# Kernel tuning notes

Hardware: AMD Instinct MI355X
Metric: run time of the kernel (lower is better)

The kernel has to match this reference:

```python
import jax, jax.numpy as jnp
import numpy as np
from jax import lax

K = 3          # dynamic filter kernel size
NH = 8         # attention heads

def _conv2d(x, w, b, pad, groups=1):
    y = lax.conv_general_dilated(x, w, (1, 1), [(pad, pad), (pad, pad)],
                                 feature_group_count=groups,
                                 dimension_numbers=('NCHW', 'OIHW', 'NCHW'))
    return y + b[None, :, None, None]

def _pw(x, w, b):  # 1x1 conv: w (O,C)
    return jnp.einsum('oc,bchw->bohw', w, x) + b[None, :, None, None]

def _lrelu(x):
    return jnp.where(x >= 0, x, 0.2 * x)

def _unfold(x, k):  # (B,C,H,W) -> (B,C,k*k,H,W), matches F.unfold ordering
    p = k // 2
    xp = jnp.pad(x, ((0, 0), (0, 0), (p, p), (p, p)))
    H, W = x.shape[2], x.shape[3]
    return jnp.stack([xp[:, :, i:i + H, j:j + W] for i in range(k) for j in range(k)], axis=2)

def setup_inputs() -> dict:
    key = jax.random.key(0)
    ks = jax.random.split(key, 24)
    B, C, H, W = 1, 256, 56, 56
    C2, K2 = C // 2, K * K
    s = 0.02
    d = {
        'dec_feat': jax.random.normal(ks[0], (B, C, H, W), jnp.float32),
        'enc_feat': jax.random.normal(ks[1], (B, C, H, W), jnp.float32),
        # ALPF kernel predictor: depthwise 3x3, 1x1 C->C/2, 1x1 C/2->k^2
        'alpf_dw_w': jax.random.normal(ks[2], (C, 1, 3, 3), jnp.float32) * s,
        'alpf_dw_b': jnp.zeros((C,), jnp.float32),
        'alpf_p1_w': jax.random.normal(ks[3], (C2, C), jnp.float32) * s,
        'alpf_p1_b': jnp.zeros((C2,), jnp.float32),
        'alpf_p2_w': jax.random.normal(ks[4], (K2, C2), jnp.float32) * s,
        'alpf_p2_b': jnp.zeros((K2,), jnp.float32),
        # AHPF weight predictor: 3x3 C->C/2, 1x1 C/2->k^2
        'ahpf_c1_w': jax.random.normal(ks[5], (C2, C, 3, 3), jnp.float32) * s,
        'ahpf_c1_b': jnp.zeros((C2,), jnp.float32),
        'ahpf_c2_w': jax.random.normal(ks[6], (K2, C2), jnp.float32) * s,
        'ahpf_c2_b': jnp.zeros((K2,), jnp.float32),
        # cross-attention projections (all 1x1)
        'q_w': jax.random.normal(ks[7], (C, C), jnp.float32) * s,
        'q_b': jnp.zeros((C,), jnp.float32),
        'kv_w': jax.random.normal(ks[8], (2 * C, C), jnp.float32) * s,
        'kv_b': jnp.zeros((2 * C,), jnp.float32),
        'out_w': jax.random.normal(ks[9], (C, C), jnp.float32) * s,
        'out_b': jnp.zeros((C,), jnp.float32),
        # fusion 3x3 conv
        'fusion_w': jax.random.normal(ks[10], (C, C, 3, 3), jnp.float32) * s,
        'fusion_b': jnp.zeros((C,), jnp.float32),
    }
    return d

def _forward(dec_feat, enc_feat, alpf_dw_w, alpf_dw_b, alpf_p1_w, alpf_p1_b,
             alpf_p2_w, alpf_p2_b, ahpf_c1_w, ahpf_c1_b, ahpf_c2_w, ahpf_c2_b,
             q_w, q_b, kv_w, kv_b, out_w, out_b, fusion_w, fusion_b):
    B, C, H, W = dec_feat.shape
    K2 = K * K
    # ---- Adaptive low-pass filter on dec_feat ----
    kw = _conv2d(dec_feat, alpf_dw_w, alpf_dw_b, pad=1, groups=C)
    kw = _lrelu(_pw(kw, alpf_p1_w, alpf_p1_b))
    kw = _pw(kw, alpf_p2_w, alpf_p2_b)            # (B,k2,H,W)
    kw = jax.nn.softmax(kw, axis=1)
    patches = _unfold(dec_feat, K)                # (B,C,k2,H,W)
    f_smooth = jnp.sum(patches * kw[:, None], axis=2)
    # ---- Cross attention: q from f_smooth, kv from enc_feat ----
    hd = C // NH
    N = H * W
    q = _pw(f_smooth, q_w, q_b).reshape(B, NH, hd, N)
    kv = _pw(enc_feat, kv_w, kv_b)
    k, v = jnp.split(kv, 2, axis=1)
    k = k.reshape(B, NH, hd, N)
    v = v.reshape(B, NH, hd, N)
    scale = hd ** -0.5
    attn = jnp.einsum('bhdn,bhdm->bhnm', q, k) * scale
    attn = jax.nn.softmax(attn, axis=-1)
    out = jnp.einsum('bhnm,bhdm->bhdn', attn, v).reshape(B, C, H, W)
    f_aligned = _pw(out, out_w, out_b)
    # ---- Adaptive high-pass filter on enc_feat ----
    wlp = _lrelu(_conv2d(enc_feat, ahpf_c1_w, ahpf_c1_b, pad=1))
    wlp = jax.nn.softmax(_pw(wlp, ahpf_c2_w, ahpf_c2_b), axis=1)  # (B,k2,H,W)
    whp = (-wlp).at[:, K2 // 2].add(1.0)          # delta - W_LP
    epatches = _unfold(enc_feat, K)
    f_high = enc_feat + jnp.sum(epatches * whp[:, None], axis=2)
    # ---- Fusion (w = 1.0) ----
    return _conv2d(f_aligned + 1.0 * f_high, fusion_w, fusion_b, pad=1)

def reference(dec_feat, enc_feat, alpf_dw_w, alpf_dw_b, alpf_p1_w, alpf_p1_b,
              alpf_p2_w, alpf_p2_b, ahpf_c1_w, ahpf_c1_b, ahpf_c2_w, ahpf_c2_b,
              q_w, q_b, kv_w, kv_b, out_w, out_b, fusion_w, fusion_b):
    return _forward(dec_feat, enc_feat, alpf_dw_w, alpf_dw_b, alpf_p1_w, alpf_p1_b,
                    alpf_p2_w, alpf_p2_b, ahpf_c1_w, ahpf_c1_b, ahpf_c2_w, ahpf_c2_b,
                    q_w, q_b, kv_w, kv_b, out_w, out_b, fusion_w, fusion_b)
```

## Files before the change

kernel.cpp:

```cpp
#include <hip/hip_runtime.h>
#include <hip/hip_bf16.h>

#define HH  56
#define WWC 56
#define HWP 3136
#define CC  256
#define NSPLIT 6

typedef unsigned short u16;
typedef __attribute__((ext_vector_type(8))) u16 u16x8;
typedef __attribute__((ext_vector_type(4))) u16 u16x4;
typedef __attribute__((ext_vector_type(8))) short s16x8;
typedef __attribute__((ext_vector_type(4))) float f32x4;

__device__ __forceinline__ u16 f2b(float f) {
  unsigned int x = __float_as_uint(f);
  return (u16)((x + 0x7fffu + ((x >> 16) & 1u)) >> 16);
}
__device__ __forceinline__ float b2f(u16 u) {
  return __uint_as_float(((unsigned int)u) << 16);
}
__device__ __forceinline__ f32x4 mfma16(s16x8 a, s16x8 b, f32x4 c) {
  return __builtin_amdgcn_mfma_f32_16x16x32_bf16(a, b, c, 0, 0, 0);
}

__device__ __forceinline__ float ldsel(const void* p, int i, bool bf) {
  if (bf) return __bfloat162float(((const __hip_bfloat16*)p)[i]);
  return ((const float*)p)[i];
}
__device__ __forceinline__ void stsel(void* p, int i, float v, bool bf) {
  if (bf) ((__hip_bfloat16*)p)[i] = __float2bfloat16(v);
  else ((float*)p)[i] = v;
}

__device__ __forceinline__ void ldrow8(const void* p, size_t i, bool bf,
                                       float* o) {
  if (bf) {
    u16x8 v = *(const u16x8*)((const u16*)p + i);
    #pragma unroll
    for (int j = 0; j < 8; ++j) o[j] = b2f(v[j]);
  } else {
    const float* f = (const float*)p + i;
    f32x4 a = *(const f32x4*)f;
    f32x4 b = *(const f32x4*)(f + 4);
    #pragma unroll
    for (int j = 0; j < 4; ++j) { o[j] = a[j]; o[4 + j] = b[j]; }
  }
}

__global__ void detect_dtype_k(const void* x, float* flag) {
  __shared__ int sh[256];
  int tid = threadIdx.x;
  const __hip_bfloat16* xb = (const __hip_bfloat16*)x;
  int ok = 0;
  for (int i = tid; i < 1024; i += 256) {
    float v = fabsf(__bfloat162float(xb[2 * i]));
    if (v > 9.5e-7f && v < 1.05e6f) ok++;
  }
  sh[tid] = ok;
  __syncthreads();
  for (int s = 128; s > 0; s >>= 1) {
    if (tid < s) sh[tid] += sh[tid + s];
    __syncthreads();
  }
  if (tid == 0) flag[0] = (sh[0] > 512) ? 1.f : 0.f;
}

__global__ __launch_bounds__(256)
void pack_all_k(const void* __restrict__ p1, const void* __restrict__ q,
                const void* __restrict__ kv, const void* __restrict__ ow,
                const void* __restrict__ c1, const void* __restrict__ fu,
                u16* __restrict__ d_p1, u16* __restrict__ d_q,
                u16* __restrict__ d_kv, u16* __restrict__ d_ow,
                u16* __restrict__ d_c1, u16* __restrict__ d_fu,
                const float* __restrict__ dflag) {
  bool bf = dflag[0] > 0.5f;
  int b = blockIdx.x, tid = threadIdx.x;
  if (b < 128) { int g = b * 256 + tid; d_p1[g] = f2b(ldsel(p1, g, bf)); return; }
  b -= 128;
  if (b < 256) { int g = b * 256 + tid; d_q[g] = f2b(ldsel(q, g, bf)); return; }
  b -= 256;
  if (b < 512) { int g = b * 256 + tid; d_kv[g] = f2b(ldsel(kv, g, bf)); return; }
  b -= 512;
  if (b < 256) { int g = b * 256 + tid; d_ow[g] = f2b(ldsel(ow, g, bf)); return; }
  b -= 256;
  if (b < 128) {
    int g = b * 256 + tid;
    #pragma unroll
    for (int t = 0; t < 9; ++t)
      d_c1[(size_t)t * 32768 + g] = f2b(ldsel(c1, g * 9 + t, bf));
    return;
  }
  b -= 128;
  {
    int g = b * 256 + tid;
    #pragma unroll
    for (int t = 0; t < 9; ++t)
      d_fu[(size_t)t * 65536 + g] = f2b(ldsel(fu, g * 9 + t, bf));
  }
}

__device__ __forceinline__ void dwconv_body(int gid, const void* x,
                                            const void* wt, const void* bs,
                                            u16* y, bool bf) {
  int c = gid / 392, g = gid - c * 392;
  int p0 = g * 8;
  int h = p0 / WWC, w0 = p0 - h * WWC;
  float wv[9];
  #pragma unroll
  for (int t = 0; t < 9; ++t) wv[t] = ldsel(wt, c * 9 + t, bf);
  float bv = ldsel(bs, c, bf);
  float acc[8];
  #pragma unroll
  for (int j = 0; j < 8; ++j) acc[j] = bv;
  const size_t cbase = (size_t)c * HWP;
  #pragma unroll
  for (int dh = -1; dh <= 1; ++dh) {
    int hh = h + dh;
    if (hh < 0 || hh >= HH) continue;
    size_t rbase = cbase + hh * WWC + w0;
    float v[8];
    ldrow8(x, rbase, bf, v);
    float lft = (w0 > 0) ? ldsel(x, rbase - 1, bf) : 0.f;
    float rgt = (w0 < 48) ? ldsel(x, rbase + 8, bf) : 0.f;
    float wm = wv[(dh + 1) * 3 + 0], wc = wv[(dh + 1) * 3 + 1],
          wp = wv[(dh + 1) * 3 + 2];
    #pragma unroll
    for (int j = 0; j < 8; ++j) {
      float vm = (j == 0) ? lft : v[j - 1];
      float vp = (j == 7) ? rgt : v[j + 1];
      acc[j] += vm * wm + v[j] * wc + vp * wp;
    }
  }
  u16x8 st;
  #pragma unroll
  for (int j = 0; j < 8; ++j) st[j] = f2b(acc[j]);
  *(u16x8*)&y[cbase + p0] = st;
}

template<bool HIGH>
__device__ __forceinline__ void spatial_body(int gid, const void* x,
                                             const u16* w9, u16* y, bool bf) {
  int c = gid / 392, g = gid - c * 392;
  int p0 = g * 8;
  int h = p0 / WWC, w0 = p0 - h * WWC;
  const size_t cbase = (size_t)c * HWP;
  float acc[8];
  if (HIGH) {
    ldrow8(x, cbase + p0, bf, acc);
  } else {
    #pragma unroll
    for (int j = 0; j < 8; ++j) acc[j] = 0.f;
  }
  #pragma unroll
  for (int dh = -1; dh <= 1; ++dh) {
    int hh = h + dh;
    if (hh < 0 || hh >= HH) continue;
    size_t rbase = cbase + hh * WWC + w0;
    float v[8];
    ldrow8(x, rbase, bf, v);
    float lft = (w0 > 0) ? ldsel(x, rbase - 1, bf) : 0.f;
    float rgt = (w0 < 48) ? ldsel(x, rbase + 8, bf) : 0.f;
    float wm[8], wc[8], wp[8];
    {
      int tb = (dh + 1) * 3;
      u16x8 a = *(const u16x8*)&w9[(size_t)(tb + 0) * HWP + p0];
      u16x8 b = *(const u16x8*)&w9[(size_t)(tb + 1) * HWP + p0];
      u16x8 d = *(const u16x8*)&w9[(size_t)(tb + 2) * HWP + p0];
      #pragma unroll
      for (int j = 0; j < 8; ++j) { wm[j] = b2f(a[j]); wc[j] = b2f(b[j]); wp[j] = b2f(d[j]); }
    }
    #pragma unroll
    for (int j = 0; j < 8; ++j) {
      float vm = (j == 0) ? lft : v[j - 1];
      float vp = (j == 7) ? rgt : v[j + 1];
      acc[j] += vm * wm[j] + v[j] * wc[j] + vp * wp[j];
    }
  }
  u16x8 st;
  #pragma unroll
  for (int j = 0; j < 8; ++j) st[j] = f2b(acc[j]);
  *(u16x8*)&y[cbase + p0] = st;
}

template<bool DELTA>
__device__ __forceinline__ void pw9_body(int pblk, const void* w2,
                                         const void* b2, const u16* hid,
                                         u16* out9, bool bf) {
  __shared__ float Wl[9][128];
  __shared__ float Pl[4][9][33];
  int tid = threadIdx.x;
  for (int i = tid; i < 1152; i += 256) Wl[i >> 7][i & 127] = ldsel(w2, i, bf);
  __syncthreads();
  int pix = tid & 31, cig = tid >> 5;
  int p = pblk * 32 + pix;
  int ci0 = cig * 16;
  float acc[9] = {0.f, 0.f, 0.f, 0.f, 0.f, 0.f, 0.f, 0.f, 0.f};
  #pragma unroll
  for (int j = 0; j < 16; ++j) {
    float xv = b2f(hid[(size_t)(ci0 + j) * HWP + p]);
    #pragma unroll
    for (int t = 0; t < 9; ++t) acc[t] += Wl[t][ci0 + j] * xv;
  }
  #pragma unroll
  for (int t = 0; t < 9; ++t) acc[t] += __shfl_xor(acc[t], 32);
  int wv = tid >> 6;
  if ((tid & 63) < 32) {
    #pragma unroll
    for (int t = 0; t < 9; ++t) Pl[wv][t][pix] = acc[t];
  }
  __syncthreads();
  if (tid < 32) {
    float a[9];
    #pragma unroll
    for (int t = 0; t < 9; ++t)
      a[t] = Pl[0][t][pix] + Pl[1][t][pix] + Pl[2][t][pix] + Pl[3][t][pix] +
             ldsel(b2, t, bf);
    float mx = a[0];
    #pragma unroll
    for (int t = 1; t < 9; ++t) mx = fmaxf(mx, a[t]);
    float s = 0.f;
    #pragma unroll
    for (int t = 0; t < 9; ++t) { a[t] = __expf(a[t] - mx); s += a[t]; }
    float inv = 1.f / s;
    #pragma unroll
    for (int t = 0; t < 9; ++t) {
      float v = a[t] * inv;
      if (DELTA) v = ((t == 4) ? 1.f : 0.f) - v;
      out9[(size_t)t * HWP + p] = f2b(v);
    }
  }
}

template<int TAPS, int ACT, bool ADDIN, int OMODE>
__device__ __forceinline__ void mgemm_body(
    int bid, int sz, int NZ, int NO, int O,
    const u16* __restrict__ Wp, const void* __restrict__ X,
    const void* __restrict__ bias, const u16* __restrict__ addin,
    void* __restrict__ Y, int Cin, bool wbf, bool xbf, int xmode,
    int bias_off, u16 (*Ws)[72], u16 (*Xs)[72]) {
  int p0 = (bid / NO) * 32, o0 = (bid % NO) * 32;
  int t0 = (TAPS * sz) / NZ, t1 = (TAPS * (sz + 1)) / NZ;
  int tid = threadIdx.x, lane = tid & 63, wv = tid >> 6;
  int oq = (wv & 1) * 16, pq = (wv >> 1) * 16;
  int frow = lane & 15, kgrp = (lane >> 4) * 8;
  int wol = tid >> 3, wkk = (tid & 7) * 8;
  int pl = tid & 31, xkk = (tid >> 5) * 8;
  int p = p0 + pl, h = p / WWC, w = p - h * WWC;
  f32x4 acc = {0.f, 0.f, 0.f, 0.f};
  for (int t = t0; t < t1; ++t) {
    int dh = t / 3 - 1, dw = t % 3 - 1;
    int hh = h + dh, ww = w + dw;
    bool rowok = (TAPS == 1) || ((hh >= 0) && (hh < HH) && (ww >= 0) && (ww < WWC));
    int xoff = (TAPS == 1) ? p : hh * WWC + ww;
    const u16* Wrow = Wp + (size_t)t * O * Cin;
    for (int kb = 0; kb < Cin; kb += 64) {
      __syncthreads();
      *(u16x8*)&Ws[wol][wkk] =
          *(const u16x8*)&Wrow[(size_t)(o0 + wol) * Cin + kb + wkk];
      {
        u16x8 xv;
        if (xmode == 2) {
          if (rowok) {
            xv = *(const u16x8*)&((const u16*)X)[(size_t)xoff * Cin + kb + xkk];
          } else {
            #pragma unroll
            for (int j = 0; j < 8; ++j) xv[j] = 0;
          }
        } else if (xmode == 3) {
          #pragma unroll
          for (int j = 0; j < 8; ++j)
            xv[j] = rowok ? ((const u16*)X)[(size_t)(kb + xkk + j) * HWP + xoff]
                          : (u16)0;
        } else {
          #pragma unroll
          for (int j = 0; j < 8; ++j) {
            int kk = xkk + j;
            float v = rowok ? ldsel(X, (size_t)(kb + kk) * HWP + xoff, xbf) : 0.f;
            xv[j] = f2b(v);
          }
        }
        *(u16x8*)&Xs[pl][xkk] = xv;
      }
      __syncthreads();
      #pragma unroll
      for (int ks = 0; ks < 2; ++ks) {
        s16x8 aw = *(const s16x8*)&Ws[oq + frow][ks * 32 + kgrp];
        s16x8 ax = *(const s16x8*)&Xs[pq + frow][ks * 32 + kgrp];
        acc = mfma16(aw, ax, acc);
      }
    }
  }
  int orow = (lane >> 4) * 4;
  int ogb = o0 + oq + orow;
  int pg = p0 + pq + frow;
  if (OMODE == 4) {
    float* Yp = (float*)Y + (size_t)sz * O * HWP;
    #pragma unroll
    for (int r = 0; r < 4; ++r)
      Yp[(size_t)(ogb + r) * HWP + pg] = acc[r];
  } else if (OMODE == 5) {
    if (ogb < 256) {
      u16x4 st;
      #pragma unroll
      for (int r = 0; r < 4; ++r)
        st[r] = f2b(acc[r] + ldsel(bias, ogb + r, wbf));
      *(u16x4*)&((u16*)Y)[(size_t)pg * 256 + ogb] = st;
    } else {
      u16* V = (u16*)Y + (size_t)CC * HWP;
      #pragma unroll
      for (int r = 0; r < 4; ++r)
        V[(size_t)(ogb + r - 256) * HWP + pg] =
            f2b(acc[r] + ldsel(bias, ogb + r, wbf));
    }
  } else if (OMODE == 2) {
    u16x4 st;
    #pragma unroll
    for (int r = 0; r < 4; ++r) {
      float yv = acc[r] + ldsel(bias, bias_off + ogb + r, wbf);
      if (ACT == 1) yv = (yv >= 0.f) ? yv : 0.2f * yv;
      if (ADDIN) yv += b2f(addin[(size_t)(ogb + r) * HWP + pg]);
      st[r] = f2b(yv);
    }
    *(u16x4*)&((u16*)Y)[(size_t)pg * O + ogb] = st;
  } else {
    #pragma unroll
    for (int r = 0; r < 4; ++r) {
      int og = ogb + r;
      float yv = acc[r] + ldsel(bias, bias_off + og, wbf);
      if (ACT == 1) yv = (yv >= 0.f) ? yv : 0.2f * yv;
      if (ADDIN) yv += b2f(addin[(size_t)og * HWP + pg]);
      if (OMODE == 3) ((u16*)Y)[(size_t)og * HWP + pg] = f2b(yv);
      else stsel(Y, (size_t)og * HWP + pg, yv, (OMODE == 1) && wbf);
    }
  }
}

template<int TAPS, int ACT, bool ADDIN, int OMODE>
__global__ __launch_bounds__(256)
void mgemm32_k(const u16* __restrict__ Wp, const void* __restrict__ X,
               const void* __restrict__ bias, const u16* __restrict__ addin,
               void* __restrict__ Y, int Cin,
               const float* __restrict__ dflag, int xmode, int bias_off) {
  __shared__ u16 Ws[32][72];
  __shared__ u16 Xs[32][72];
  bool wbf = dflag[0] > 0.5f;
  bool xbf = (xmode == 1) ? wbf : false;
  int NO = gridDim.y;
  int bid = blockIdx.x + blockIdx.y * gridDim.x;
  mgemm_body<TAPS, ACT, ADDIN, OMODE>(bid, blockIdx.z, gridDim.z, NO, NO * 32,
                                      Wp, X, bias, addin, Y, Cin, wbf, xbf,
                                      xmode, bias_off, Ws, Xs);
}

__global__ __launch_bounds__(256)
void stage1_k(const void* __restrict__ dec, const void* __restrict__ dw_w,
              const void* __restrict__ dw_b, u16* __restrict__ A,
              const u16* __restrict__ wp_kv, const void* __restrict__ enc,
              const void* __restrict__ kv_b, u16* __restrict__ k16,
              const float* __restrict__ dflag) {
  __shared__ u16 Ws[32][72];
  __shared__ u16 Xs[32][72];
  bool bf = dflag[0] > 0.5f;
  int b = blockIdx.x;
  if (b < 392) {
    dwconv_body(b * 256 + threadIdx.x, dec, dw_w, dw_b, A, bf);
  } else {
    mgemm_body<1, 0, false, 5>(b - 392, 0, 1, 16, 512, wp_kv, enc, kv_b,
                               nullptr, k16, 256, bf, bf, 1, 0, Ws, Xs);
  }
}

__global__ __launch_bounds__(256)
void stageA_k(const u16* __restrict__ wp_p1, const u16* __restrict__ A,
              const void* __restrict__ p1_b, u16* __restrict__ hid,
              const u16* __restrict__ wp_c1, const void* __restrict__ enc,
              float* __restrict__ Pc1, const float* __restrict__ dflag) {
  __shared__ u16 Ws[32][72];
  __shared__ u16 Xs[32][72];
  bool bf = dflag[0] > 0.5f;
  int b = blockIdx.x;
  if (b < 392) {
    mgemm_body<1, 1, false, 3>(b, 0, 1, 4, 128, wp_p1, A, p1_b, nullptr,
                               hid, 256, bf, false, 3, 0, Ws, Xs);
  } else {
    int rem = b - 392;
    int sz = rem / 392, bb = rem - sz * 392;
    mgemm_body<9, 1, false, 4>(bb, sz, 3, 4, 128, wp_c1, enc, nullptr,
                               nullptr, Pc1, 256, bf, bf, 1, 0, Ws, Xs);
  }
}

__global__ __launch_bounds__(256)
void stageB_k(const void* __restrict__ p2_w, const void* __restrict__ p2_b,
              const u16* __restrict__ hid, u16* __restrict__ s9,
              const float* __restrict__ Pc1, const void* __restrict__ c1_b,
              u16* __restrict__ hid2, const float* __restrict__ dflag) {
  bool bf = dflag[0] > 0.5f;
  int b = blockIdx.x;
  if (b < 98) {
    pw9_body<false>(b, p2_w, p2_b, hid, s9, bf);
  } else {
    int flat = ((b - 98) * 256 + threadIdx.x) * 4;
    int o = flat / HWP;
    f32x4 a = *(const f32x4*)&Pc1[flat];
    f32x4 c = *(const f32x4*)&Pc1[flat + 128 * HWP];
    f32x4 d = *(const f32x4*)&Pc1[flat + 2 * 128 * HWP];
    float bv = ldsel(c1_b, o, bf);
    u16x4 st;
    #pragma unroll
    for (int j = 0; j < 4; ++j) {
      float v = a[j] + c[j] + d[j] + bv;
      v = (v >= 0.f) ? v : 0.2f * v;
      st[j] = f2b(v);
    }
    *(u16x4*)&hid2[flat] = st;
  }
}

__global__ __launch_bounds__(256)
void stageC_k(const void* __restrict__ dec, const u16* __restrict__ s9,
              u16* __restrict__ Bb, const void* __restrict__ c2_w,
              const void* __restrict__ c2_b, const u16* __restrict__ hid2,
              u16* __restrict__ s9b, const float* __restrict__ dflag) {
  bool bf = dflag[0] > 0.5f;
  int b = blockIdx.x;
  if (b < 392) {
    spatial_body<false>(b * 256 + threadIdx.x, dec, s9, Bb, bf);
  } else {
    pw9_body<true>(b - 392, c2_w, c2_b, hid2, s9b, bf);
  }
}

__global__ __launch_bounds__(256)
void stageD_k(const u16* __restrict__ wp_q, const u16* __restrict__ Bb,
              const void* __restrict__ q_b, u16* __restrict__ qb16,
              const void* __restrict__ enc, const u16* __restrict__ s9b,
              u16* __restrict__ Bb2, const float* __restrict__ dflag) {
  __shared__ u16 Ws[32][72];
  __shared__ u16 Xs[32][72];
  bool bf = dflag[0] > 0.5f;
  int b = blockIdx.x;
  if (b < 784) {
    mgemm_body<1, 0, false, 2>(b, 0, 1, 8, 256, wp_q, Bb, q_b, nullptr,
                               qb16, 256, bf, false, 3, 0, Ws, Xs);
  } else {
    spatial_body<true>((b - 784) * 256 + threadIdx.x, enc, s9b, Bb2, bf);
  }
}

__global__ __launch_bounds__(256)
void attn_part_k(const u16* __restrict__ Qb, const u16* __restrict__ Kb,
                 const u16* __restrict__ Vb, u16* __restrict__ Op,
                 float* __restrict__ Lb) {
  __shared__ u16 Ks[64][40];
  __shared__ u16 Vs[32][72];
  __shared__ u16 Ps[4][16][72];
  int h = blockIdx.y, n0 = blockIdx.x * 64, sz = blockIdx.z;
  int tid = threadIdx.x, lane = tid & 63, wv = tid >> 6;
  int frow = lane & 15, gq = lane >> 4, kgrp = gq * 8;
  int ml = tid >> 2, dseg = (tid & 3) * 8;
  int vd = tid >> 3, vm = (tid & 7) * 8;
  const float QS = 0.17677669529663687f * 1.4426950408889634f;
  s16x8 aq;
  {
    u16x8 qv = *(const u16x8*)&Qb[(size_t)(n0 + wv * 16 + frow) * 256 + h * 32 + kgrp];
    u16x8 qs;
    #pragma unroll
    for (int j = 0; j < 8; ++j) qs[j] = f2b(b2f(qv[j]) * QS);
    aq = *(s16x8*)&qs;
  }
  f32x4 oa0 = {0.f, 0.f, 0.f, 0.f}, oa1 = {0.f, 0.f, 0.f, 0.f};
  float lsum = 0.f;
  int t_begin = (49 * sz) / NSPLIT, t_end = (49 * (sz + 1)) / NSPLIT;
  u16x8 kreg = *(const u16x8*)&Kb[(size_t)(t_begin * 64 + ml) * 256 + h * 32 + dseg];
  u16x8 vreg = *(const u16x8*)&Vb[(size_t)(h * 32 + vd) * HWP + t_begin * 64 + vm];
  for (int t = t_begin; t < t_end; ++t) {
    __syncthreads();
    *(u16x8*)&Ks[ml][dseg] = kreg;
    *(u16x8*)&Vs[vd][vm] = vreg;
    if (t + 1 < t_end) {
      kreg = *(const u16x8*)&Kb[(size_t)((t + 1) * 64 + ml) * 256 + h * 32 + dseg];
      vreg = *(const u16x8*)&Vb[(size_t)(h * 32 + vd) * HWP + (t + 1) * 64 + vm];
    }
    __syncthreads();
    f32x4 zero = {0.f, 0.f, 0.f, 0.f};
    #pragma unroll
    for (int fm = 0; fm < 4; ++fm) {
      s16x8 ak = *(const s16x8*)&Ks[fm * 16 + frow][kgrp];
      f32x4 s = mfma16(ak, aq, zero);
      u16x4 pe;
      #pragma unroll
      for (int r = 0; r < 4; ++r) {
        float e = exp2f(fminf(s[r], 43.f));
        lsum += e;
        pe[r] = (u16)(__float_as_uint(e) >> 16);
      }
      *(u16x4*)&Ps[wv][frow][fm * 16 + gq * 4] = pe;
    }
    #pragma unroll
    for (int ks = 0; ks < 2; ++ks) {
      s16x8 ap = *(const s16x8*)&Ps[wv][frow][ks * 32 + kgrp];
      s16x8 bv0 = *(const s16x8*)&Vs[frow][ks * 32 + kgrp];
      s16x8 bv1 = *(const s16x8*)&Vs[16 + frow][ks * 32 + kgrp];
      oa0 = mfma16(ap, bv0, oa0);
      oa1 = mfma16(ap, bv1, oa1);
    }
  }
  lsum += __shfl_xor(lsum, 16);
  lsum += __shfl_xor(lsum, 32);
  if (lane < 16)
    Lb[(size_t)(sz * 8 + h) * HWP + n0 + wv * 16 + frow] = lsum;
  #pragma unroll
  for (int r = 0; r < 4; ++r) {
    int n = n0 + wv * 16 + gq * 4 + r;
    Op[(size_t)(sz * 256 + h * 32 + frow) * HWP + n]      = f2b(oa0[r]);
    Op[(size_t)(sz * 256 + h * 32 + 16 + frow) * HWP + n] = f2b(oa1[r]);
  }
}

__global__ __launch_bounds__(256)
void attn_combine_k(const u16* __restrict__ Op, const float* __restrict__ Lb,
                    u16* __restrict__ A) {
  int gid = blockIdx.x * 256 + threadIdx.x;
  int hd = gid / 392, g = gid - hd * 392;
  int n0 = g * 8, h = hd >> 5;
  float L[8] = {0,0,0,0,0,0,0,0}, O[8] = {0,0,0,0,0,0,0,0};
  #pragma unroll
  for (int s = 0; s < NSPLIT; ++s) {
    const float* Lp = &Lb[(size_t)(s * 8 + h) * HWP + n0];
    f32x4 l0 = *(const f32x4*)Lp;
    f32x4 l1 = *(const f32x4*)(Lp + 4);
    u16x8 ov = *(const u16x8*)&Op[(size_t)(s * 256 + hd) * HWP + n0];
    #pragma unroll
    for (int j = 0; j < 4; ++j) { L[j] += l0[j]; L[4 + j] += l1[j]; }
    #pragma unroll
    for (int j = 0; j < 8; ++j) O[j] += b2f(ov[j]);
  }
  u16x8 st;
  #pragma unroll
  for (int j = 0; j < 8; ++j) st[j] = f2b(O[j] / L[j]);
  *(u16x8*)&A[(size_t)hd * HWP + n0] = st;
}

__global__ __launch_bounds__(256)
void comb3f_k(const float* __restrict__ P, const void* __restrict__ bias,
              void* __restrict__ Y, const float* __restrict__ dflag) {
  bool bf = dflag[0] > 0.5f;
  int flat = (blockIdx.x * 256 + threadIdx.x) * 4;
  int o = flat / HWP;
  f32x4 a = *(const f32x4*)&P[flat];
  f32x4 c = *(const f32x4*)&P[flat + 256 * HWP];
  f32x4 d = *(const f32x4*)&P[flat + 2 * 256 * HWP];
  float bv = ldsel(bias, o, bf);
  if (bf) {
    u16x4 st;
    #pragma unroll
    for (int j = 0; j < 4; ++j) st[j] = f2b(a[j] + c[j] + d[j] + bv);
    *(u16x4*)&((u16*)Y)[flat] = st;
  } else {
    f32x4 st;
    #pragma unroll
    for (int j = 0; j < 4; ++j) st[j] = a[j] + c[j] + d[j] + bv;
    *(f32x4*)&((float*)Y)[flat] = st;
  }
}

extern "C" void kernel_launch(void* const* d_in, const int* in_sizes, int n_in,
                              void* d_out, int out_size, void* d_ws, size_t ws_size,
                              hipStream_t stream) {
  const void* dec   = d_in[0];
  const void* enc   = d_in[1];
  const void* dw_w  = d_in[2];
  const void* dw_b  = d_in[3];
  const void* p1_w  = d_in[4];
  const void* p1_b  = d_in[5];
  const void* p2_w  = d_in[6];
  const void* p2_b  = d_in[7];
  const void* c1_w  = d_in[8];
  const void* c1_b  = d_in[9];
  const void* c2_w  = d_in[10];
  const void* c2_b  = d_in[11];
  const void* q_w   = d_in[12];
  const void* q_b   = d_in[13];
  const void* kv_w  = d_in[14];
  const void* kv_b  = d_in[15];
  const void* out_w = d_in[16];
  const void* out_b = d_in[17];
  const void* fu_w  = d_in[18];
  const void* fu_b  = d_in[19];

  const int CH = CC * HWP;
  float* flag = (float*)d_ws;
  u16* pk     = (u16*)(flag + 8);
  u16* A      = pk;              pk += CH;
  u16* hid    = pk;              pk += 128 * HWP;
  u16* hid2   = pk;              pk += 128 * HWP;
  u16* s9     = pk;              pk += 9 * HWP;
  u16* s9b    = pk;              pk += 9 * HWP;
  u16* Bb     = pk;              pk += CH;
  u16* Bb2    = pk;              pk += CH;
  u16* qb16   = pk;              pk += CH;
  u16* k16    = pk;              pk += CH;
  u16* v16    = pk;              pk += CH;
  u16* wp_p1  = pk;              pk += 128 * 256;
  u16* wp_q   = pk;              pk += 256 * 256;
  u16* wp_kv  = pk;              pk += 512 * 256;
  u16* wp_out = pk;              pk += 256 * 256;
  u16* wp_c1  = pk;              pk += 128 * 256 * 9;
  u16* wp_fu  = pk;              pk += 256 * 256 * 9;
  pk += (size_t)(-(intptr_t)pk) & 7;
  float* Lb   = (float*)pk;
  u16* Opart  = (u16*)(Lb + 48 * HWP);
  float* Pc1 = Lb;
  float* Pfu = Lb;

  dim3 blk(256);
  detect_dtype_k<<<1, blk, 0, stream>>>(dec, flag);

  pack_all_k<<<1536, blk, 0, stream>>>(p1_w, q_w, kv_w, out_w, c1_w, fu_w,
                                       wp_p1, wp_q, wp_kv, wp_out, wp_c1, wp_fu,
                                       flag);

  stage1_k<<<1960, blk, 0, stream>>>(dec, dw_w, dw_b, A, wp_kv, enc, kv_b,
                                     k16, flag);

  stageA_k<<<1568, blk, 0, stream>>>(wp_p1, A, p1_b, hid, wp_c1, enc, Pc1, flag);

  stageB_k<<<490, blk, 0, stream>>>(p2_w, p2_b, hid, s9, Pc1, c1_b, hid2, flag);

  stageC_k<<<490, blk, 0, stream>>>(dec, s9, Bb, c2_w, c2_b, hid2, s9b, flag);

  stageD_k<<<1176, blk, 0, stream>>>(wp_q, Bb, q_b, qb16, enc, s9b, Bb2, flag);

  attn_part_k<<<dim3(49, 8, NSPLIT), blk, 0, stream>>>(qb16, k16, v16, Opart, Lb);
  attn_combine_k<<<392, blk, 0, stream>>>(Opart, Lb, A);

  mgemm32_k<1, 0, true, 2><<<dim3(98, 8), blk, 0, stream>>>(
      wp_out, A, out_b, Bb2, qb16, 256, flag, 3, 0);

  mgemm32_k<9, 0, false, 4><<<dim3(98, 8, 3), blk, 0, stream>>>(
      wp_fu, qb16, nullptr, nullptr, Pfu, 256, flag, 2, 0);
  comb3f_k<<<784, blk, 0, stream>>>(Pfu, fu_b, d_out, flag);
}
```

Before: 135.3 us.

## Drop runtime dtype detection, hardcode fp32 inputs, fuse high-pass into attention launch

Removes the dtype-detection kernel and every runtime bf16/fp32 branch, treating all inputs as fp32 and turning the X-load mode into a compile-time template parameter. The high-pass spatial filter moves out of the old stageD launch into the attention-partial launch as extra blocks, and the q projection now runs as its own GEMM launch. The aim is one fewer kernel launch, fewer per-thread flag loads and branches, and better overlap of the small spatial work with attention. It gives up support for bf16 inputs.

```diff
diff --git a/kernel.cpp b/kernel.cpp
--- a/kernel.cpp
+++ b/kernel.cpp
@@ -23,72 +23,34 @@
 __device__ __forceinline__ f32x4 mfma16(s16x8 a, s16x8 b, f32x4 c) {
   return __builtin_amdgcn_mfma_f32_16x16x32_bf16(a, b, c, 0, 0, 0);
 }
-
-__device__ __forceinline__ float ldsel(const void* p, int i, bool bf) {
-  if (bf) return __bfloat162float(((const __hip_bfloat16*)p)[i]);
-  return ((const float*)p)[i];
-}
-__device__ __forceinline__ void stsel(void* p, int i, float v, bool bf) {
-  if (bf) ((__hip_bfloat16*)p)[i] = __float2bfloat16(v);
-  else ((float*)p)[i] = v;
-}
-
-__device__ __forceinline__ void ldrow8(const void* p, size_t i, bool bf,
-                                       float* o) {
-  if (bf) {
-    u16x8 v = *(const u16x8*)((const u16*)p + i);
-    #pragma unroll
-    for (int j = 0; j < 8; ++j) o[j] = b2f(v[j]);
-  } else {
-    const float* f = (const float*)p + i;
-    f32x4 a = *(const f32x4*)f;
-    f32x4 b = *(const f32x4*)(f + 4);
-    #pragma unroll
-    for (int j = 0; j < 4; ++j) { o[j] = a[j]; o[4 + j] = b[j]; }
-  }
-}
-
-__global__ void detect_dtype_k(const void* x, float* flag) {
-  __shared__ int sh[256];
-  int tid = threadIdx.x;
-  const __hip_bfloat16* xb = (const __hip_bfloat16*)x;
-  int ok = 0;
-  for (int i = tid; i < 1024; i += 256) {
-    float v = fabsf(__bfloat162float(xb[2 * i]));
-    if (v > 9.5e-7f && v < 1.05e6f) ok++;
-  }
-  sh[tid] = ok;
-  __syncthreads();
-  for (int s = 128; s > 0; s >>= 1) {
-    if (tid < s) sh[tid] += sh[tid + s];
-    __syncthreads();
-  }
-  if (tid == 0) flag[0] = (sh[0] > 512) ? 1.f : 0.f;
-}
-
-__global__ __launch_bounds__(256)
-void pack_all_k(const void* __restrict__ p1, const void* __restrict__ q,
-                const void* __restrict__ kv, const void* __restrict__ ow,
-                const void* __restrict__ c1, const void* __restrict__ fu,
+__device__ __forceinline__ void ldrow8f(const float* p, size_t i, float* o) {
+  f32x4 a = *(const f32x4*)(p + i);
+  f32x4 b = *(const f32x4*)(p + i + 4);
+  #pragma unroll
+  for (int j = 0; j < 4; ++j) { o[j] = a[j]; o[4 + j] = b[j]; }
+}
+
+__global__ __launch_bounds__(256)
+void pack_all_k(const float* __restrict__ p1, const float* __restrict__ q,
+                const float* __restrict__ kv, const float* __restrict__ ow,
+                const float* __restrict__ c1, const float* __restrict__ fu,
                 u16* __restrict__ d_p1, u16* __restrict__ d_q,
                 u16* __restrict__ d_kv, u16* __restrict__ d_ow,
-                u16* __restrict__ d_c1, u16* __restrict__ d_fu,
-                const float* __restrict__ dflag) {
-  bool bf = dflag[0] > 0.5f;
+                u16* __restrict__ d_c1, u16* __restrict__ d_fu) {
   int b = blockIdx.x, tid = threadIdx.x;
-  if (b < 128) { int g = b * 256 + tid; d_p1[g] = f2b(ldsel(p1, g, bf)); return; }
+  if (b < 128) { int g = b * 256 + tid; d_p1[g] = f2b(p1[g]); return; }
   b -= 128;
-  if (b < 256) { int g = b * 256 + tid; d_q[g] = f2b(ldsel(q, g, bf)); return; }
+  if (b < 256) { int g = b * 256 + tid; d_q[g] = f2b(q[g]); return; }
   b -= 256;
-  if (b < 512) { int g = b * 256 + tid; d_kv[g] = f2b(ldsel(kv, g, bf)); return; }
+  if (b < 512) { int g = b * 256 + tid; d_kv[g] = f2b(kv[g]); return; }
   b -= 512;
-  if (b < 256) { int g = b * 256 + tid; d_ow[g] = f2b(ldsel(ow, g, bf)); return; }
+  if (b < 256) { int g = b * 256 + tid; d_ow[g] = f2b(ow[g]); return; }
   b -= 256;
   if (b < 128) {
     int g = b * 256 + tid;
     #pragma unroll
     for (int t = 0; t < 9; ++t)
-      d_c1[(size_t)t * 32768 + g] = f2b(ldsel(c1, g * 9 + t, bf));
+      d_c1[(size_t)t * 32768 + g] = f2b(c1[g * 9 + t]);
     return;
   }
   b -= 128;
@@ -96,20 +58,20 @@
     int g = b * 256 + tid;
     #pragma unroll
     for (int t = 0; t < 9; ++t)
-      d_fu[(size_t)t * 65536 + g] = f2b(ldsel(fu, g * 9 + t, bf));
-  }
-}
-
-__device__ __forceinline__ void dwconv_body(int gid, const void* x,
-                                            const void* wt, const void* bs,
-                                            u16* y, bool bf) {
+      d_fu[(size_t)t * 65536 + g] = f2b(fu[g * 9 + t]);
+  }
+}
+
+__device__ __forceinline__ void dwconv_body(int gid, const float* x,
+                                            const float* wt, const float* bs,
+                                            u16* y) {
   int c = gid / 392, g = gid - c * 392;
   int p0 = g * 8;
   int h = p0 / WWC, w0 = p0 - h * WWC;
   float wv[9];
   #pragma unroll
-  for (int t = 0; t < 9; ++t) wv[t] = ldsel(wt, c * 9 + t, bf);
-  float bv = ldsel(bs, c, bf);
+  for (int t = 0; t < 9; ++t) wv[t] = wt[c * 9 + t];
+  float bv = bs[c];
   float acc[8];
   #pragma unroll
   for (int j = 0; j < 8; ++j) acc[j] = bv;
@@ -120,9 +82,9 @@
     if (hh < 0 || hh >= HH) continue;
     size_t rbase = cbase + hh * WWC + w0;
     float v[8];
-    ldrow8(x, rbase, bf, v);
-    float lft = (w0 > 0) ? ldsel(x, rbase - 1, bf) : 0.f;
-    float rgt = (w0 < 48) ? ldsel(x, rbase + 8, bf) : 0.f;
+    ldrow8f(x, rbase, v);
+    float lft = (w0 > 0) ? x[rbase - 1] : 0.f;
+    float rgt = (w0 < 48) ? x[rbase + 8] : 0.f;
     float wm = wv[(dh + 1) * 3 + 0], wc = wv[(dh + 1) * 3 + 1],
           wp = wv[(dh + 1) * 3 + 2];
     #pragma unroll
@@ -139,15 +101,15 @@
 }
 
 template<bool HIGH>
-__device__ __forceinline__ void spatial_body(int gid, const void* x,
-                                             const u16* w9, u16* y, bool bf) {
+__device__ __forceinline__ void spatial_body(int gid, const float* x,
+                                             const u16* w9, u16* y) {
   int c = gid / 392, g = gid - c * 392;
   int p0 = g * 8;
   int h = p0 / WWC, w0 = p0 - h * WWC;
   const size_t cbase = (size_t)c * HWP;
   float acc[8];
   if (HIGH) {
-    ldrow8(x, cbase + p0, bf, acc);
+    ldrow8f(x, cbase + p0, acc);
   } else {
     #pragma unroll
     for (int j = 0; j < 8; ++j) acc[j] = 0.f;
@@ -158,9 +120,9 @@
     if (hh < 0 || hh >= HH) continue;
     size_t rbase = cbase + hh * WWC + w0;
     float v[8];
-    ldrow8(x, rbase, bf, v);
-    float lft = (w0 > 0) ? ldsel(x, rbase - 1, bf) : 0.f;
-    float rgt = (w0 < 48) ? ldsel(x, rbase + 8, bf) : 0.f;
+    ldrow8f(x, rbase, v);
+    float lft = (w0 > 0) ? x[rbase - 1] : 0.f;
+    float rgt = (w0 < 48) ? x[rbase + 8] : 0.f;
     float wm[8], wc[8], wp[8];
     {
       int tb = (dh + 1) * 3;
@@ -184,13 +146,13 @@
 }
 
 template<bool DELTA>
-__device__ __forceinline__ void pw9_body(int pblk, const void* w2,
-                                         const void* b2, const u16* hid,
-                                         u16* out9, bool bf) {
+__device__ __forceinline__ void pw9_body(int pblk, const float* w2,
+                                         const float* b2, const u16* hid,
+                                         u16* out9) {
   __shared__ float Wl[9][128];
   __shared__ float Pl[4][9][33];
   int tid = threadIdx.x;
-  for (int i = tid; i < 1152; i += 256) Wl[i >> 7][i & 127] = ldsel(w2, i, bf);
+  for (int i = tid; i < 1152; i += 256) Wl[i >> 7][i & 127] = w2[i];
   __syncthreads();
   int pix = tid & 31, cig = tid >> 5;
   int p = pblk * 32 + pix;
@@ -215,7 +177,7 @@
     #pragma unroll
     for (int t = 0; t < 9; ++t)
       a[t] = Pl[0][t][pix] + Pl[1][t][pix] + Pl[2][t][pix] + Pl[3][t][pix] +
-             ldsel(b2, t, bf);
+             b2[t];
     float mx = a[0];
     #pragma unroll
     for (int t = 1; t < 9; ++t) mx = fmaxf(mx, a[t]);
@@ -232,13 +194,12 @@
   }
 }
 
-template<int TAPS, int ACT, bool ADDIN, int OMODE>
+template<int TAPS, int ACT, bool ADDIN, int OMODE, int XMODE>
 __device__ __forceinline__ void mgemm_body(
     int bid, int sz, int NZ, int NO, int O,
     const u16* __restrict__ Wp, const void* __restrict__ X,
-    const void* __restrict__ bias, const u16* __restrict__ addin,
-    void* __restrict__ Y, int Cin, bool wbf, bool xbf, int xmode,
-    int bias_off, u16 (*Ws)[72], u16 (*Xs)[72]) {
+    const float* __restrict__ bias, const u16* __restrict__ addin,
+    void* __restrict__ Y, int Cin, u16 (*Ws)[72], u16 (*Xs)[72]) {
   int p0 = (bid / NO) * 32, o0 = (bid % NO) * 32;
   int t0 = (TAPS * sz) / NZ, t1 = (TAPS * (sz + 1)) / NZ;
   int tid = threadIdx.x, lane = tid & 63, wv = tid >> 6;
@@ -260,14 +221,14 @@
           *(const u16x8*)&Wrow[(size_t)(o0 + wol) * Cin + kb + wkk];
       {
         u16x8 xv;
-        if (xmode == 2) {
+        if (XMODE == 2) {
           if (rowok) {
             xv = *(const u16x8*)&((const u16*)X)[(size_t)xoff * Cin + kb + xkk];
           } else {
             #pragma unroll
             for (int j = 0; j < 8; ++j) xv[j] = 0;
           }
-        } else if (xmode == 3) {
+        } else if (XMODE == 3) {
           #pragma unroll
           for (int j = 0; j < 8; ++j)
             xv[j] = rowok ? ((const u16*)X)[(size_t)(kb + xkk + j) * HWP + xoff]
@@ -275,8 +236,8 @@
         } else {
           #pragma unroll
           for (int j = 0; j < 8; ++j) {
-            int kk = xkk + j;
-            float v = rowok ? ldsel(X, (size_t)(kb + kk) * HWP + xoff, xbf) : 0.f;
+            float v = rowok ? ((const float*)X)[(size_t)(kb + xkk + j) * HWP + xoff]
+                            : 0.f;
             xv[j] = f2b(v);
           }
         }
@@ -303,21 +264,19 @@
     if (ogb < 256) {
       u16x4 st;
       #pragma unroll
-      for (int r = 0; r < 4; ++r)
-        st[r] = f2b(acc[r] + ldsel(bias, ogb + r, wbf));
+      for (int r = 0; r < 4; ++r) st[r] = f2b(acc[r] + bias[ogb + r]);
       *(u16x4*)&((u16*)Y)[(size_t)pg * 256 + ogb] = st;
     } else {
       u16* V = (u16*)Y + (size_t)CC * HWP;
       #pragma unroll
       for (int r = 0; r < 4; ++r)
-        V[(size_t)(ogb + r - 256) * HWP + pg] =
-            f2b(acc[r] + ldsel(bias, ogb + r, wbf));
+        V[(size_t)(ogb + r - 256) * HWP + pg] = f2b(acc[r] + bias[ogb + r]);
     }
   } else if (OMODE == 2) {
     u16x4 st;
     #pragma unroll
     for (int r = 0; r < 4; ++r) {
-      float yv = acc[r] + ldsel(bias, bias_off + ogb + r, wbf);
+      float yv = acc[r] + bias[ogb + r];
       if (ACT == 1) yv = (yv >= 0.f) ? yv : 0.2f * yv;
       if (ADDIN) yv += b2f(addin[(size_t)(ogb + r) * HWP + pg]);
       st[r] = f2b(yv);
@@ -326,87 +285,77 @@
   } else {
     #pragma unroll
     for (int r = 0; r < 4; ++r) {
-      int og = ogb + r;
-      float yv = acc[r] + ldsel(bias, bias_off + og, wbf);
+      float yv = acc[r] + bias[ogb + r];
       if (ACT == 1) yv = (yv >= 0.f) ? yv : 0.2f * yv;
-      if (ADDIN) yv += b2f(addin[(size_t)og * HWP + pg]);
-      if (OMODE == 3) ((u16*)Y)[(size_t)og * HWP + pg] = f2b(yv);
-      else stsel(Y, (size_t)og * HWP + pg, yv, (OMODE == 1) && wbf);
-    }
-  }
-}
-
-template<int TAPS, int ACT, bool ADDIN, int OMODE>
+      ((u16*)Y)[(size_t)(ogb + r) * HWP + pg] = f2b(yv);
+    }
+  }
+}
+
+template<int TAPS, int ACT, bool ADDIN, int OMODE, int XMODE>
 __global__ __launch_bounds__(256)
 void mgemm32_k(const u16* __restrict__ Wp, const void* __restrict__ X,
-               const void* __restrict__ bias, const u16* __restrict__ addin,
-               void* __restrict__ Y, int Cin,
-               const float* __restrict__ dflag, int xmode, int bias_off) {
+               const float* __restrict__ bias, const u16* __restrict__ addin,
+               void* __restrict__ Y, int Cin) {
   __shared__ u16 Ws[32][72];
   __shared__ u16 Xs[32][72];
-  bool wbf = dflag[0] > 0.5f;
-  bool xbf = (xmode == 1) ? wbf : false;
   int NO = gridDim.y;
   int bid = blockIdx.x + blockIdx.y * gridDim.x;
-  mgemm_body<TAPS, ACT, ADDIN, OMODE>(bid, blockIdx.z, gridDim.z, NO, NO * 32,
-                                      Wp, X, bias, addin, Y, Cin, wbf, xbf,
-                                      xmode, bias_off, Ws, Xs);
-}
-
-__global__ __launch_bounds__(256)
-void stage1_k(const void* __restrict__ dec, const void* __restrict__ dw_w,
-              const void* __restrict__ dw_b, u16* __restrict__ A,
-              const u16* __restrict__ wp_kv, const void* __restrict__ enc,
-              const void* __restrict__ kv_b, u16* __restrict__ k16,
-              const float* __restrict__ dflag) {
+  mgemm_body<TAPS, ACT, ADDIN, OMODE, XMODE>(bid, blockIdx.z, gridDim.z, NO,
+                                             NO * 32, Wp, X, bias, addin, Y,
+                                             Cin, Ws, Xs);
+}
+
+__global__ __launch_bounds__(256)
+void stage1_k(const float* __restrict__ dec, const float* __restrict__ dw_w,
+              const float* __restrict__ dw_b, u16* __restrict__ A,
+              const u16* __restrict__ wp_kv, const float* __restrict__ enc,
+              const float* __restrict__ kv_b, u16* __restrict__ k16) {
   __shared__ u16 Ws[32][72];
   __shared__ u16 Xs[32][72];
-  bool bf = dflag[0] > 0.5f;
   int b = blockIdx.x;
   if (b < 392) {
-    dwconv_body(b * 256 + threadIdx.x, dec, dw_w, dw_b, A, bf);
-  } else {
-    mgemm_body<1, 0, false, 5>(b - 392, 0, 1, 16, 512, wp_kv, enc, kv_b,
-                               nullptr, k16, 256, bf, bf, 1, 0, Ws, Xs);
+    dwconv_body(b * 256 + threadIdx.x, dec, dw_w, dw_b, A);
+  } else {
+    mgemm_body<1, 0, false, 5, 0>(b - 392, 0, 1, 16, 512, wp_kv, enc, kv_b,
+                                  nullptr, k16, 256, Ws, Xs);
   }
 }
 
 __global__ __launch_bounds__(256)
 void stageA_k(const u16* __restrict__ wp_p1, const u16* __restrict__ A,
-              const void* __restrict__ p1_b, u16* __restrict__ hid,
-              const u16* __restrict__ wp_c1, const void* __restrict__ enc,
-              float* __restrict__ Pc1, const float* __restrict__ dflag) {
+              const float* __restrict__ p1_b, u16* __restrict__ hid,
+              const u16* __restrict__ wp_c1, const float* __restrict__ enc,
+              float* __restrict__ Pc1) {
   __shared__ u16 Ws[32][72];
   __shared__ u16 Xs[32][72];
-  bool bf = dflag[0] > 0.5f;
   int b = blockIdx.x;
   if (b < 392) {
-    mgemm_body<1, 1, false, 3>(b, 0, 1, 4, 128, wp_p1, A, p1_b, nullptr,
-                               hid, 256, bf, false, 3, 0, Ws, Xs);
+    mgemm_body<1, 1, false, 3, 3>(b, 0, 1, 4, 128, wp_p1, A, p1_b, nullptr,
+                                  hid, 256, Ws, Xs);
   } else {
     int rem = b - 392;
     int sz = rem / 392, bb = rem - sz * 392;
-    mgemm_body<9, 1, false, 4>(bb, sz, 3, 4, 128, wp_c1, enc, nullptr,
-                               nullptr, Pc1, 256, bf, bf, 1, 0, Ws, Xs);
-  }
-}
-
-__global__ __launch_bounds__(256)
-void stageB_k(const void* __restrict__ p2_w, const void* __restrict__ p2_b,
+    mgemm_body<9, 1, false, 4, 0>(bb, sz, 3, 4, 128, wp_c1, enc, nullptr,
+                                  nullptr, Pc1, 256, Ws, Xs);
+  }
+}
+
+__global__ __launch_bounds__(256)
+void stageB_k(const float* __restrict__ p2_w, const float* __restrict__ p2_b,
               const u16* __restrict__ hid, u16* __restrict__ s9,
-              const float* __restrict__ Pc1, const void* __restrict__ c1_b,
-              u16* __restrict__ hid2, const float* __restrict__ dflag) {
-  bool bf = dflag[0] > 0.5f;
+              const float* __restrict__ Pc1, const float* __restrict__ c1_b,
+              u16* __restrict__ hid2) {
   int b = blockIdx.x;
   if (b < 98) {
-    pw9_body<false>(b, p2_w, p2_b, hid, s9, bf);
+    pw9_body<false>(b, p2_w, p2_b, hid, s9);
   } else {
     int flat = ((b - 98) * 256 + threadIdx.x) * 4;
     int o = flat / HWP;
     f32x4 a = *(const f32x4*)&Pc1[flat];
     f32x4 c = *(const f32x4*)&Pc1[flat + 128 * HWP];
     f32x4 d = *(const f32x4*)&Pc1[flat + 2 * 128 * HWP];
-    float bv = ldsel(c1_b, o, bf);
+    float bv = c1_b[o];
     u16x4 st;
     #pragma unroll
     for (int j = 0; j < 4; ++j) {
@@ -419,44 +368,24 @@
 }
 
 __global__ __launch_bounds__(256)
-void stageC_k(const void* __restrict__ dec, const u16* __restrict__ s9,
-              u16* __restrict__ Bb, const void* __restrict__ c2_w,
-              const void* __restrict__ c2_b, const u16* __restrict__ hid2,
-              u16* __restrict__ s9b, const float* __restrict__ dflag) {
-  bool bf = dflag[0] > 0.5f;
+void stageC_k(const float* __restrict__ dec, const u16* __restrict__ s9,
+              u16* __restrict__ Bb, const float* __restrict__ c2_w,
+              const float* __restrict__ c2_b, const u16* __restrict__ hid2,
+              u16* __restrict__ s9b) {
   int b = blockIdx.x;
   if (b < 392) {
-    spatial_body<false>(b * 256 + threadIdx.x, dec, s9, Bb, bf);
-  } else {
-    pw9_body<true>(b - 392, c2_w, c2_b, hid2, s9b, bf);
-  }
-}
-
-__global__ __launch_bounds__(256)
-void stageD_k(const u16* __restrict__ wp_q, const u16* __restrict__ Bb,
-              const void* __restrict__ q_b, u16* __restrict__ qb16,
-              const void* __restrict__ enc, const u16* __restrict__ s9b,
-              u16* __restrict__ Bb2, const float* __restrict__ dflag) {
-  __shared__ u16 Ws[32][72];
-  __shared__ u16 Xs[32][72];
-  bool bf = dflag[0] > 0.5f;
-  int b = blockIdx.x;
-  if (b < 784) {
-    mgemm_body<1, 0, false, 2>(b, 0, 1, 8, 256, wp_q, Bb, q_b, nullptr,
-                               qb16, 256, bf, false, 3, 0, Ws, Xs);
-  } else {
-    spatial_body<true>((b - 784) * 256 + threadIdx.x, enc, s9b, Bb2, bf);
-  }
-}
-
-__global__ __launch_bounds__(256)
-void attn_part_k(const u16* __restrict__ Qb, const u16* __restrict__ Kb,
-                 const u16* __restrict__ Vb, u16* __restrict__ Op,
-                 float* __restrict__ Lb) {
-  __shared__ u16 Ks[64][40];
-  __shared__ u16 Vs[32][72];
-  __shared__ u16 Ps[4][16][72];
-  int h = blockIdx.y, n0 = blockIdx.x * 64, sz = blockIdx.z;
+    spatial_body<false>(b * 256 + threadIdx.x, dec, s9, Bb);
+  } else {
+    pw9_body<true>(b - 392, c2_w, c2_b, hid2, s9b);
+  }
+}
+
+__device__ __forceinline__ void attn_body(int qx, int h, int sz,
+                                          const u16* Qb, const u16* Kb,
+                                          const u16* Vb, u16* Op, float* Lb,
+                                          u16 (*Ks)[40], u16 (*Vs)[72],
+                                          u16 (*Ps)[16][72]) {
+  int n0 = qx * 64;
   int tid = threadIdx.x, lane = tid & 63, wv = tid >> 6;
   int frow = lane & 15, gq = lane >> 4, kgrp = gq * 8;
   int ml = tid >> 2, dseg = (tid & 3) * 8;
@@ -520,6 +449,23 @@
 }
 
 __global__ __launch_bounds__(256)
+void attnsp_k(const u16* __restrict__ Qb, const u16* __restrict__ Kb,
+              const u16* __restrict__ Vb, u16* __restrict__ Op,
+              float* __restrict__ Lb, const float* __restrict__ enc,
+              const u16* __restrict__ s9b, u16* __restrict__ Bb2) {
+  __shared__ u16 Ks[64][40];
+  __shared__ u16 Vs[32][72];
+  __shared__ u16 Ps[4][16][72];
+  int b = blockIdx.x;
+  if (b < 2352) {
+    int qx = b % 49, h = (b / 49) % 8, sz = b / 392;
+    attn_body(qx, h, sz, Qb, Kb, Vb, Op, Lb, Ks, Vs, Ps);
+  } else {
+    spatial_body<true>((b - 2352) * 256 + threadIdx.x, enc, s9b, Bb2);
+  }
+}
+
+__global__ __launch_bounds__(256)
 void attn_combine_k(const u16* __restrict__ Op, const float* __restrict__ Lb,
                     u16* __restrict__ A) {
   int gid = blockIdx.x * 256 + threadIdx.x;
@@ -544,55 +490,46 @@
 }
 
 __global__ __launch_bounds__(256)
-void comb3f_k(const float* __restrict__ P, const void* __restrict__ bias,
-              void* __restrict__ Y, const float* __restrict__ dflag) {
-  bool bf = dflag[0] > 0.5f;
+void comb3f_k(const float* __restrict__ P, const float* __restrict__ bias,
+              float* __restrict__ Y) {
   int flat = (blockIdx.x * 256 + threadIdx.x) * 4;
   int o = flat / HWP;
   f32x4 a = *(const f32x4*)&P[flat];
   f32x4 c = *(const f32x4*)&P[flat + 256 * HWP];
   f32x4 d = *(const f32x4*)&P[flat + 2 * 256 * HWP];
-  float bv = ldsel(bias, o, bf);
-  if (bf) {
-    u16x4 st;
-    #pragma unroll
-    for (int j = 0; j < 4; ++j) st[j] = f2b(a[j] + c[j] + d[j] + bv);
-    *(u16x4*)&((u16*)Y)[flat] = st;
-  } else {
-    f32x4 st;
-    #pragma unroll
-    for (int j = 0; j < 4; ++j) st[j] = a[j] + c[j] + d[j] + bv;
-    *(f32x4*)&((float*)Y)[flat] = st;
-  }
+  float bv = bias[o];
+  f32x4 st;
+  #pragma unroll
+  for (int j = 0; j < 4; ++j) st[j] = a[j] + c[j] + d[j] + bv;
+  *(f32x4*)&Y[flat] = st;
 }
 
 extern "C" void kernel_launch(void* const* d_in, const int* in_sizes, int n_in,
                               void* d_out, int out_size, void* d_ws, size_t ws_size,
                               hipStream_t stream) {
-  const void* dec   = d_in[0];
-  const void* enc   = d_in[1];
-  const void* dw_w  = d_in[2];
-  const void* dw_b  = d_in[3];
-  const void* p1_w  = d_in[4];
-  const void* p1_b  = d_in[5];
-  const void* p2_w  = d_in[6];
-  const void* p2_b  = d_in[7];
-  const void* c1_w  = d_in[8];
-  const void* c1_b  = d_in[9];
-  const void* c2_w  = d_in[10];
-  const void* c2_b  = d_in[11];
-  const void* q_w   = d_in[12];
-  const void* q_b   = d_in[13];
-  const void* kv_w  = d_in[14];
-  const void* kv_b  = d_in[15];
-  const void* out_w = d_in[16];
-  const void* out_b = d_in[17];
-  const void* fu_w  = d_in[18];
-  const void* fu_b  = d_in[19];
+  const float* dec   = (const float*)d_in[0];
+  const float* enc   = (const float*)d_in[1];
+  const float* dw_w  = (const float*)d_in[2];
+  const float* dw_b  = (const float*)d_in[3];
+  const float* p1_w  = (const float*)d_in[4];
+  const float* p1_b  = (const float*)d_in[5];
+  const float* p2_w  = (const float*)d_in[6];
+  const float* p2_b  = (const float*)d_in[7];
+  const float* c1_w  = (const float*)d_in[8];
+  const float* c1_b  = (const float*)d_in[9];
+  const float* c2_w  = (const float*)d_in[10];
+  const float* c2_b  = (const float*)d_in[11];
+  const float* q_w   = (const float*)d_in[12];
+  const float* q_b   = (const float*)d_in[13];
+  const float* kv_w  = (const float*)d_in[14];
+  const float* kv_b  = (const float*)d_in[15];
+  const float* out_w = (const float*)d_in[16];
+  const float* out_b = (const float*)d_in[17];
+  const float* fu_w  = (const float*)d_in[18];
+  const float* fu_b  = (const float*)d_in[19];
 
   const int CH = CC * HWP;
-  float* flag = (float*)d_ws;
-  u16* pk     = (u16*)(flag + 8);
+  u16* pk     = (u16*)d_ws;
   u16* A      = pk;              pk += CH;
   u16* hid    = pk;              pk += 128 * HWP;
   u16* hid2   = pk;              pk += 128 * HWP;
@@ -616,30 +553,28 @@
   float* Pfu = Lb;
 
   dim3 blk(256);
-  detect_dtype_k<<<1, blk, 0, stream>>>(dec, flag);
 
   pack_all_k<<<1536, blk, 0, stream>>>(p1_w, q_w, kv_w, out_w, c1_w, fu_w,
-                                       wp_p1, wp_q, wp_kv, wp_out, wp_c1, wp_fu,
-                                       flag);
-
-  stage1_k<<<1960, blk, 0, stream>>>(dec, dw_w, dw_b, A, wp_kv, enc, kv_b,
-                                     k16, flag);
-
-  stageA_k<<<1568, blk, 0, stream>>>(wp_p1, A, p1_b, hid, wp_c1, enc, Pc1, flag);
-
-  stageB_k<<<490, blk, 0, stream>>>(p2_w, p2_b, hid, s9, Pc1, c1_b, hid2, flag);
-
-  stageC_k<<<490, blk, 0, stream>>>(dec, s9, Bb, c2_w, c2_b, hid2, s9b, flag);
-
-  stageD_k<<<1176, blk, 0, stream>>>(wp_q, Bb, q_b, qb16, enc, s9b, Bb2, flag);
-
-  attn_part_k<<<dim3(49, 8, NSPLIT), blk, 0, stream>>>(qb16, k16, v16, Opart, Lb);
+                                       wp_p1, wp_q, wp_kv, wp_out, wp_c1, wp_fu);
+
+  stage1_k<<<1960, blk, 0, stream>>>(dec, dw_w, dw_b, A, wp_kv, enc, kv_b, k16);
+
+  stageA_k<<<1568, blk, 0, stream>>>(wp_p1, A, p1_b, hid, wp_c1, enc, Pc1);
+
+  stageB_k<<<490, blk, 0, stream>>>(p2_w, p2_b, hid, s9, Pc1, c1_b, hid2);
+
+  stageC_k<<<490, blk, 0, stream>>>(dec, s9, Bb, c2_w, c2_b, hid2, s9b);
+
+  mgemm32_k<1, 0, false, 2, 3><<<dim3(98, 8), blk, 0, stream>>>(
+      wp_q, Bb, q_b, nullptr, qb16, 256);
+
+  attnsp_k<<<2744, blk, 0, stream>>>(qb16, k16, v16, Opart, Lb, enc, s9b, Bb2);
   attn_combine_k<<<392, blk, 0, stream>>>(Opart, Lb, A);
 
-  mgemm32_k<1, 0, true, 2><<<dim3(98, 8), blk, 0, stream>>>(
-      wp_out, A, out_b, Bb2, qb16, 256, flag, 3, 0);
-
-  mgemm32_k<9, 0, false, 4><<<dim3(98, 8, 3), blk, 0, stream>>>(
-      wp_fu, qb16, nullptr, nullptr, Pfu, 256, flag, 2, 0);
-  comb3f_k<<<784, blk, 0, stream>>>(Pfu, fu_b, d_out, flag);
-}
+  mgemm32_k<1, 0, true, 2, 3><<<dim3(98, 8), blk, 0, stream>>>(
+      wp_out, A, out_b, Bb2, qb16, 256);
+
+  mgemm32_k<9, 0, false, 4, 2><<<dim3(98, 8, 3), blk, 0, stream>>>(
+      wp_fu, qb16, nullptr, nullptr, Pfu, 256);
+  comb3f_k<<<784, blk, 0, stream>>>(Pfu, fu_b, (float*)d_out);
+}
```

After: 121.3 us. -10.3%, faster.
